# Kernel tuning notes

Measured on AMD Instinct MI355X. Metric: run time of the kernel, lower is better.

The kernel has to match this reference:

```python
import jax, jax.numpy as jnp
import numpy as np

D_MODEL, D_STATE, D_CONV, EXPAND = 1024, 64, 4, 2
D_INNER = D_MODEL * EXPAND
BATCH, SEQ = 4, 4096


def setup_inputs() -> dict:
    key = jax.random.key(0)
    ks = jax.random.split(key, 9)
    s = lambda fan_in: 1.0 / np.sqrt(fan_in)
    return {
        "x": jax.random.normal(ks[0], (BATCH, SEQ, D_MODEL), jnp.float32),
        "in_proj_w": jax.random.uniform(ks[1], (D_MODEL, 2 * D_INNER), jnp.float32, -s(D_MODEL), s(D_MODEL)),
        "conv_w": jax.random.uniform(ks[2], (D_INNER, 1, D_CONV), jnp.float32, -s(D_CONV), s(D_CONV)),
        "conv_b": jax.random.uniform(ks[3], (D_INNER,), jnp.float32, -s(D_CONV), s(D_CONV)),
        "sB_w": jax.random.uniform(ks[4], (D_INNER, D_STATE), jnp.float32, -s(D_INNER), s(D_INNER)),
        "sC_w": jax.random.uniform(ks[5], (D_INNER, D_STATE), jnp.float32, -s(D_INNER), s(D_INNER)),
        "sdelta_w": jax.random.uniform(ks[6], (D_INNER, D_INNER), jnp.float32, -s(D_INNER), s(D_INNER)),
        "sdelta_b": jax.random.uniform(ks[7], (D_INNER,), jnp.float32, -s(D_INNER), s(D_INNER)),
        "A_log": jnp.log(jnp.arange(1, D_STATE + 1, dtype=jnp.float32)),
        "D_param": jnp.ones((D_INNER,), jnp.float32),
        "out_proj_w": jax.random.uniform(ks[8], (D_INNER, D_MODEL), jnp.float32, -s(D_INNER), s(D_INNER)),
        "out_proj_b": jnp.zeros((D_MODEL,), jnp.float32),
    }


def reference(x, in_proj_w, conv_w, conv_b, sB_w, sC_w, sdelta_w, sdelta_b, A_log, D_param, out_proj_w, out_proj_b):
    batch, seq_len, _ = x.shape
    d_inner = conv_w.shape[0]
    k = conv_w.shape[-1]
    # input projection + gate split
    x_proj = x @ in_proj_w                         # (B, L, 2*Di)
    x_ssm, x_gate = jnp.split(x_proj, 2, axis=-1)
    # causal depthwise conv1d: torch pads (k-1) both sides then truncates to L == left-pad only
    xc = jnp.transpose(x_ssm, (0, 2, 1))           # (B, Di, L)
    xc = jax.lax.conv_general_dilated(
        xc, conv_w, window_strides=(1,), padding=[(k - 1, 0)],
        dimension_numbers=("NCH", "OIH", "NCH"), feature_group_count=d_inner)
    xc = xc + conv_b[None, :, None]
    xc = jax.nn.silu(jnp.transpose(xc, (0, 2, 1)))  # (B, L, Di)
    # selection mechanism
    A = -jnp.exp(A_log)                            # (N,)
    Bm = xc @ sB_w                                 # (B, L, N)
    Cm = xc @ sC_w                                 # (B, L, N)
    delta = jax.nn.softplus(xc @ sdelta_w + sdelta_b)  # (B, L, Di)
    # selective scan over time with lax.scan
    def step(h, inp):
        xt, dt, Bt, Ct = inp                       # (B,Di),(B,Di),(B,N),(B,N)
        Abar = jnp.exp(dt[..., None] * A)          # (B, Di, N)
        h = Abar * h + (dt * xt)[..., None] * Bt[:, None, :]
        y = jnp.einsum("bdn,bn->bd", h, Ct)
        return h, y
    h0 = jnp.zeros((batch, d_inner, A.shape[0]), x.dtype)
    xs = (jnp.swapaxes(xc, 0, 1), jnp.swapaxes(delta, 0, 1),
          jnp.swapaxes(Bm, 0, 1), jnp.swapaxes(Cm, 0, 1))
    _, ys = jax.lax.scan(step, h0, xs)             # (L, B, Di)
    y = jnp.swapaxes(ys, 0, 1) + xc * D_param      # skip via D
    y = y * jax.nn.silu(x_gate)                    # gating
    return y @ out_proj_w + out_proj_b             # (B, L, d_model)
```

## Files before the change

kernel.cpp:

```cpp
#include <hip/hip_runtime.h>
#include <math.h>


typedef __bf16 bf16;
typedef __attribute__((__ext_vector_type__(8))) __bf16 bf16x8;
typedef __attribute__((__ext_vector_type__(4))) __bf16 bf16x4;
typedef __attribute__((__ext_vector_type__(4))) float  f32x4;

#define DM     1024
#define DI     2048
#define NPROJ  4096
#define LSEQ   4096
#define NB     4
#define NS     64
#define NCH    32
#define TC     128

#define LDT 72

__global__ __launch_bounds__(256) void transpose_w(const float* __restrict__ in,
                                                   bf16* __restrict__ out,
                                                   int R, int C) {
  __shared__ float tile[32][33];
  int bc = blockIdx.x * 32, br = blockIdx.y * 32;
  int tx = threadIdx.x & 31, ty = threadIdx.x >> 5;
#pragma unroll
  for (int i = 0; i < 32; i += 8)
    tile[ty + i][tx] = in[(size_t)(br + ty + i) * C + bc + tx];
  __syncthreads();
#pragma unroll
  for (int i = 0; i < 32; i += 8)
    out[(size_t)(bc + ty + i) * R + br + tx] = (bf16)tile[tx][ty + i];
}

template <int EPI, int ADT>
__global__ __launch_bounds__(256) void gemm_bt(const void* __restrict__ Ap,
                                               const bf16* __restrict__ Wt,
                                               const float* __restrict__ bias,
                                               void* __restrict__ Cp,
                                               void* __restrict__ Cp2,
                                               int M, int N, int Nsplit, int K) {
  __shared__ __align__(16) bf16 As[128 * LDT];
  __shared__ __align__(16) bf16 Bs[128 * LDT];
  const int tid = threadIdx.x;
  const int m0 = blockIdx.x * 128, n0 = blockIdx.y * 128;
  const int wave = tid >> 6, lane = tid & 63;
  const int wm = (wave & 1) * 64, wn = (wave >> 1) * 64;
  const int lr = lane & 15, lq = lane >> 4;

  f32x4 acc[4][4];
  const f32x4 z4 = {0.f, 0.f, 0.f, 0.f};
#pragma unroll
  for (int i = 0; i < 4; i++)
#pragma unroll
    for (int j = 0; j < 4; j++) acc[i][j] = z4;

  for (int k0 = 0; k0 < K; k0 += 64) {
    if (ADT == 1) {
      const float* A = (const float*)Ap;
#pragma unroll
      for (int it = 0; it < 8; it++) {
        int e = tid + it * 256;
        int row = e >> 4, col4 = (e & 15) * 4;
        float4 v = *(const float4*)&A[(size_t)(m0 + row) * K + k0 + col4];
        bf16x4 t = {(bf16)v.x, (bf16)v.y, (bf16)v.z, (bf16)v.w};
        *(bf16x4*)&As[row * LDT + col4] = t;
      }
    } else {
      const bf16* A = (const bf16*)Ap;
#pragma unroll
      for (int it = 0; it < 4; it++) {
        int e = tid + it * 256;
        int row = e >> 3, col8 = (e & 7) * 8;
        bf16x8 v = *(const bf16x8*)&A[(size_t)(m0 + row) * K + k0 + col8];
        *(bf16x8*)&As[row * LDT + col8] = v;
      }
    }
#pragma unroll
    for (int it = 0; it < 4; it++) {
      int e = tid + it * 256;
      int row = e >> 3, col8 = (e & 7) * 8;
      bf16x8 v = *(const bf16x8*)&Wt[(size_t)(n0 + row) * K + k0 + col8];
      *(bf16x8*)&Bs[row * LDT + col8] = v;
    }
    __syncthreads();
#pragma unroll
    for (int kk = 0; kk < 64; kk += 32) {
      bf16x8 af[4], bfr[4];
#pragma unroll
      for (int i = 0; i < 4; i++)
        af[i] = *(const bf16x8*)&As[(wm + i * 16 + lr) * LDT + kk + lq * 8];
#pragma unroll
      for (int j = 0; j < 4; j++)
        bfr[j] = *(const bf16x8*)&Bs[(wn + j * 16 + lr) * LDT + kk + lq * 8];
#pragma unroll
      for (int i = 0; i < 4; i++)
#pragma unroll
        for (int j = 0; j < 4; j++)
          acc[i][j] = __builtin_amdgcn_mfma_f32_16x16x32_bf16(af[i], bfr[j],
                                                              acc[i][j], 0, 0, 0);
    }
    __syncthreads();
  }

#pragma unroll
  for (int i = 0; i < 4; i++) {
#pragma unroll
    for (int j = 0; j < 4; j++) {
#pragma unroll
      for (int r = 0; r < 4; r++) {
        int row = m0 + wm + i * 16 + lq * 4 + r;
        int col = n0 + wn + j * 16 + lr;
        float v = acc[i][j][r];
        if (EPI == 0) {
          if (col < Nsplit)
            ((bf16*)Cp)[(size_t)row * Nsplit + col] = (bf16)v;
          else
            ((bf16*)Cp2)[(size_t)row * (N - Nsplit) + (col - Nsplit)] = (bf16)v;
        } else if (EPI == 1) {
          v += bias[col];
          v = (v > 20.f) ? v : log1pf(__expf(v));
          ((bf16*)Cp)[(size_t)row * N + col] = (bf16)v;
        } else if (EPI == 2) {
          ((float*)Cp)[(size_t)row * N + col] = v;
        } else {
          v += bias[col];
          ((float*)Cp)[(size_t)row * N + col] = v;
        }
      }
    }
  }
}

__global__ __launch_bounds__(256) void conv_silu(const bf16* __restrict__ xssm,
                                                 const float* __restrict__ w,
                                                 const float* __restrict__ cb,
                                                 bf16* __restrict__ xc) {
  size_t idx = (size_t)blockIdx.x * 256 + threadIdx.x;
  int d = (int)(idx & (DI - 1));
  size_t bt = idx >> 11;
  int t = (int)(bt & (LSEQ - 1));
  const float4 wv = *(const float4*)&w[d * 4];
  float acc = cb[d];
  const bf16* base = xssm + bt * DI + d;
  if (t >= 3) acc += (float)base[-3 * DI] * wv.x;
  if (t >= 2) acc += (float)base[-2 * DI] * wv.y;
  if (t >= 1) acc += (float)base[-1 * DI] * wv.z;
  acc += (float)base[0] * wv.w;
  acc = acc / (1.f + __expf(-acc));
  xc[idx] = (bf16)acc;
}

__global__ __launch_bounds__(256) void scan_pass1(const bf16* __restrict__ delta,
                                                  const bf16* __restrict__ xc,
                                                  const float* __restrict__ BC,
                                                  float* __restrict__ S,
                                                  float* __restrict__ SD) {
  __shared__ __align__(16) float Bsh[64][64];
  const int b = blockIdx.z, c = blockIdx.y, d = blockIdx.x * 256 + threadIdx.x;
  const int tid = threadIdx.x;
  float h[NS];
#pragma unroll
  for (int n = 0; n < NS; n++) h[n] = 0.f;
  float sumdt = 0.f;

  for (int half = 0; half < 2; half++) {
    const int tbase = c * TC + half * 64;
    __syncthreads();
#pragma unroll
    for (int it = 0; it < 4; it++) {
      int e = tid + it * 256;
      int tt = e >> 4, n4 = (e & 15) * 4;
      *(float4*)&Bsh[tt][n4] =
          *(const float4*)&BC[((size_t)b * LSEQ + tbase + tt) * 128 + n4];
    }
    __syncthreads();
    for (int tt = 0; tt < 64; tt++) {
      size_t o = ((size_t)b * LSEQ + tbase + tt) * DI + d;
      float dt = (float)delta[o];
      float xv = (float)xc[o];
      float dx = dt * xv;
      float r = __expf(-dt);
      sumdt += dt;
      float rp = r;
#pragma unroll
      for (int n4 = 0; n4 < 16; n4++) {
        float4 Bv = *(const float4*)&Bsh[tt][n4 * 4];
        h[n4 * 4 + 0] = rp * h[n4 * 4 + 0] + dx * Bv.x; rp *= r;
        h[n4 * 4 + 1] = rp * h[n4 * 4 + 1] + dx * Bv.y; rp *= r;
        h[n4 * 4 + 2] = rp * h[n4 * 4 + 2] + dx * Bv.z; rp *= r;
        h[n4 * 4 + 3] = rp * h[n4 * 4 + 3] + dx * Bv.w; rp *= r;
      }
    }
  }
  size_t sb = (((size_t)b * NCH + c) * NS) * DI + d;
#pragma unroll
  for (int n = 0; n < NS; n++) S[sb + (size_t)n * DI] = h[n];
  SD[((size_t)b * NCH + c) * DI + d] = sumdt;
}

__global__ __launch_bounds__(256) void scan_pass2(float* __restrict__ S,
                                                  const float* __restrict__ SD) {
  const int d = blockIdx.x * 256 + threadIdx.x;
  const int n = blockIdx.y, b = blockIdx.z;
  const float nf = -(float)(n + 1);
  float h = 0.f;
  for (int c = 0; c < NCH; c++) {
    size_t o = (((size_t)b * NCH + c) * NS + n) * DI + d;
    float s = S[o];
    S[o] = h;
    float sd = SD[((size_t)b * NCH + c) * DI + d];
    h = __expf(nf * sd) * h + s;
  }
}

__global__ __launch_bounds__(256) void scan_pass3(const bf16* __restrict__ delta,
                                                  const bf16* __restrict__ xc,
                                                  const float* __restrict__ BC,
                                                  const float* __restrict__ Hin,
                                                  const bf16* __restrict__ xgate,
                                                  const float* __restrict__ Dp,
                                                  bf16* __restrict__ yg) {
  __shared__ __align__(16) float Bsh[64][64];
  __shared__ __align__(16) float Csh[64][64];
  const int b = blockIdx.z, c = blockIdx.y, d = blockIdx.x * 256 + threadIdx.x;
  const int tid = threadIdx.x;
  float h[NS];
  size_t hb = (((size_t)b * NCH + c) * NS) * DI + d;
#pragma unroll
  for (int n = 0; n < NS; n++) h[n] = Hin[hb + (size_t)n * DI];
  const float Dv = Dp[d];

  for (int half = 0; half < 2; half++) {
    const int tbase = c * TC + half * 64;
    __syncthreads();
#pragma unroll
    for (int it = 0; it < 4; it++) {
      int e = tid + it * 256;
      int tt = e >> 4, n4 = (e & 15) * 4;
      size_t rowo = ((size_t)b * LSEQ + tbase + tt) * 128;
      *(float4*)&Bsh[tt][n4] = *(const float4*)&BC[rowo + n4];
      *(float4*)&Csh[tt][n4] = *(const float4*)&BC[rowo + 64 + n4];
    }
    __syncthreads();
    for (int tt = 0; tt < 64; tt++) {
      size_t row = (size_t)b * LSEQ + tbase + tt;
      size_t o = row * DI + d;
      float dt = (float)delta[o];
      float xv = (float)xc[o];
      float dx = dt * xv;
      float r = __expf(-dt);
      float rp = r;
      float y = 0.f;
#pragma unroll
      for (int n4 = 0; n4 < 16; n4++) {
        float4 Bv = *(const float4*)&Bsh[tt][n4 * 4];
        float4 Cv = *(const float4*)&Csh[tt][n4 * 4];
        h[n4 * 4 + 0] = rp * h[n4 * 4 + 0] + dx * Bv.x; y += h[n4 * 4 + 0] * Cv.x; rp *= r;
        h[n4 * 4 + 1] = rp * h[n4 * 4 + 1] + dx * Bv.y; y += h[n4 * 4 + 1] * Cv.y; rp *= r;
        h[n4 * 4 + 2] = rp * h[n4 * 4 + 2] + dx * Bv.z; y += h[n4 * 4 + 2] * Cv.z; rp *= r;
        h[n4 * 4 + 3] = rp * h[n4 * 4 + 3] + dx * Bv.w; y += h[n4 * 4 + 3] * Cv.w; rp *= r;
      }
      y += xv * Dv;
      float g = (float)xgate[o];
      y *= g / (1.f + __expf(-g));
      yg[o] = (bf16)y;
    }
  }
}

extern "C" void kernel_launch(void* const* d_in, const int* in_sizes, int n_in,
                              void* d_out, int out_size, void* d_ws, size_t ws_size,
                              hipStream_t stream) {
  const float* x         = (const float*)d_in[0];
  const float* in_proj_w = (const float*)d_in[1];
  const float* conv_w    = (const float*)d_in[2];
  const float* conv_b    = (const float*)d_in[3];
  const float* sB_w      = (const float*)d_in[4];
  const float* sC_w      = (const float*)d_in[5];
  const float* sdelta_w  = (const float*)d_in[6];
  const float* sdelta_b  = (const float*)d_in[7];
  const float* D_param    = (const float*)d_in[9];
  const float* out_proj_w = (const float*)d_in[10];
  const float* out_proj_b = (const float*)d_in[11];
  float* out = (float*)d_out;

  char* ws = (char*)d_ws;
  size_t off = 0;
  auto alloc = [&](size_t bytes) {
    char* p = ws + off;
    off += (bytes + 255) & ~(size_t)255;
    return p;
  };
  bf16* W1t  = (bf16*)alloc((size_t)NPROJ * DM * 2);
  bf16* Wdt  = (bf16*)alloc((size_t)DI * DI * 2);
  bf16* WBCt = (bf16*)alloc((size_t)128 * DI * 2);
  bf16* Wot  = (bf16*)alloc((size_t)DM * DI * 2);
  const size_t weight_bytes = off;

  const size_t PB = (size_t)LSEQ * DI * 2
                  + (size_t)LSEQ * DI * 2
                  + (size_t)LSEQ * DI * 2
                  + (size_t)LSEQ * DI * 2
                  + (size_t)LSEQ * 128 * 4
                  + (size_t)NCH * NS * DI * 4
                  + (size_t)NCH * DI * 4
                  + 8 * 256;
  int G = (ws_size >= weight_bytes + 4 * PB) ? 4
        : (ws_size >= weight_bytes + 2 * PB) ? 2 : 1;

  bf16*  xssm  = (bf16*)alloc((size_t)G * LSEQ * DI * 2);
  bf16*  xgate = (bf16*)alloc((size_t)G * LSEQ * DI * 2);
  bf16*  xc    = (bf16*)alloc((size_t)G * LSEQ * DI * 2);
  bf16*  delta = (bf16*)alloc((size_t)G * LSEQ * DI * 2);
  float* BC    = (float*)alloc((size_t)G * LSEQ * 128 * 4);
  float* S     = (float*)alloc((size_t)G * NCH * NS * DI * 4);
  float* SD    = (float*)alloc((size_t)G * NCH * DI * 4);
  bf16*  yg    = xssm;

  transpose_w<<<dim3(NPROJ / 32, DM / 32), 256, 0, stream>>>(in_proj_w, W1t, DM, NPROJ);
  transpose_w<<<dim3(DI / 32, DI / 32), 256, 0, stream>>>(sdelta_w, Wdt, DI, DI);
  transpose_w<<<dim3(NS / 32, DI / 32), 256, 0, stream>>>(sB_w, WBCt, DI, NS);
  transpose_w<<<dim3(NS / 32, DI / 32), 256, 0, stream>>>(sC_w, WBCt + (size_t)NS * DI, DI, NS);
  transpose_w<<<dim3(DM / 32, DI / 32), 256, 0, stream>>>(out_proj_w, Wot, DI, DM);

  const int M = G * LSEQ;
  for (int g = 0; g < NB / G; g++) {
    const float* xg_in = x + (size_t)g * G * LSEQ * DM;
    float* out_g = out + (size_t)g * G * LSEQ * DM;

    gemm_bt<0, 1><<<dim3(M / 128, NPROJ / 128), 256, 0, stream>>>(
        xg_in, W1t, nullptr, xssm, xgate, M, NPROJ, DI, DM);
    conv_silu<<<((size_t)M * DI) / 256, 256, 0, stream>>>(xssm, conv_w, conv_b, xc);
    gemm_bt<1, 0><<<dim3(M / 128, DI / 128), 256, 0, stream>>>(
        xc, Wdt, sdelta_b, delta, nullptr, M, DI, DI, DI);
    gemm_bt<2, 0><<<dim3(M / 128, 1), 256, 0, stream>>>(
        xc, WBCt, nullptr, BC, nullptr, M, 128, 128, DI);
    scan_pass1<<<dim3(DI / 256, NCH, G), 256, 0, stream>>>(delta, xc, BC, S, SD);
    scan_pass2<<<dim3(DI / 256, NS, G), 256, 0, stream>>>(S, SD);
    scan_pass3<<<dim3(DI / 256, NCH, G), 256, 0, stream>>>(delta, xc, BC, S, xgate,
                                                           D_param, yg);
    gemm_bt<3, 0><<<dim3(M / 128, DM / 128), 256, 0, stream>>>(
        yg, Wot, out_proj_b, out_g, nullptr, M, DM, DM, DI);
  }
}
```

Measured before the change: 1.595 ms.

## Use direct global-to-LDS loads in GEMM, fuse delta/BC GEMMs, restructure scan decay

GEMM tile loads now go through global_load_lds straight into unpadded LDS, so the register round-trip is gone. The input x is first cast to bf16 by a separate kernel, which lets every GEMM share one bf16 A path. The delta and B/C projection GEMMs are merged into a single launch with a split epilogue (softplus to bf16 for delta, fp32 for BC). In the scan kernels the serial decay-power chain is replaced by precomputed powers stepped by r^8, and the y reduction uses four accumulators to shorten dependency chains. The unpadded LDS layout may cause bank conflicts on the fragment reads, and the extra cast pass adds memory traffic.

```diff
diff --git a/kernel.cpp b/kernel.cpp
--- a/kernel.cpp
+++ b/kernel.cpp
@@ -16,7 +16,19 @@
 #define NCH    32
 #define TC     128
 
-#define LDT 72
+__device__ __forceinline__ void gl_lds16(const bf16* g, bf16* l) {
+  __builtin_amdgcn_global_load_lds(
+      (const __attribute__((address_space(1))) void*)g,
+      (__attribute__((address_space(3))) void*)l, 16, 0, 0);
+}
+
+__global__ __launch_bounds__(256) void cast_bf16(const float* __restrict__ in,
+                                                 bf16* __restrict__ out) {
+  size_t i = ((size_t)blockIdx.x * 256 + threadIdx.x) * 4;
+  float4 v = *(const float4*)&in[i];
+  bf16x4 t = {(bf16)v.x, (bf16)v.y, (bf16)v.z, (bf16)v.w};
+  *(bf16x4*)&out[i] = t;
+}
 
 __global__ __launch_bounds__(256) void transpose_w(const float* __restrict__ in,
                                                    bf16* __restrict__ out,
@@ -33,15 +45,15 @@
     out[(size_t)(bc + ty + i) * R + br + tx] = (bf16)tile[tx][ty + i];
 }
 
-template <int EPI, int ADT>
-__global__ __launch_bounds__(256) void gemm_bt(const void* __restrict__ Ap,
+template <int EPI>
+__global__ __launch_bounds__(256) void gemm_bt(const bf16* __restrict__ A,
                                                const bf16* __restrict__ Wt,
                                                const float* __restrict__ bias,
                                                void* __restrict__ Cp,
                                                void* __restrict__ Cp2,
                                                int M, int N, int Nsplit, int K) {
-  __shared__ __align__(16) bf16 As[128 * LDT];
-  __shared__ __align__(16) bf16 Bs[128 * LDT];
+  __shared__ __align__(16) bf16 As[128 * 64];
+  __shared__ __align__(16) bf16 Bs[128 * 64];
   const int tid = threadIdx.x;
   const int m0 = blockIdx.x * 128, n0 = blockIdx.y * 128;
   const int wave = tid >> 6, lane = tid & 63;
@@ -56,32 +68,13 @@
     for (int j = 0; j < 4; j++) acc[i][j] = z4;
 
   for (int k0 = 0; k0 < K; k0 += 64) {
-    if (ADT == 1) {
-      const float* A = (const float*)Ap;
-#pragma unroll
-      for (int it = 0; it < 8; it++) {
-        int e = tid + it * 256;
-        int row = e >> 4, col4 = (e & 15) * 4;
-        float4 v = *(const float4*)&A[(size_t)(m0 + row) * K + k0 + col4];
-        bf16x4 t = {(bf16)v.x, (bf16)v.y, (bf16)v.z, (bf16)v.w};
-        *(bf16x4*)&As[row * LDT + col4] = t;
-      }
-    } else {
-      const bf16* A = (const bf16*)Ap;
-#pragma unroll
-      for (int it = 0; it < 4; it++) {
-        int e = tid + it * 256;
-        int row = e >> 3, col8 = (e & 7) * 8;
-        bf16x8 v = *(const bf16x8*)&A[(size_t)(m0 + row) * K + k0 + col8];
-        *(bf16x8*)&As[row * LDT + col8] = v;
-      }
-    }
 #pragma unroll
     for (int it = 0; it < 4; it++) {
-      int e = tid + it * 256;
-      int row = e >> 3, col8 = (e & 7) * 8;
-      bf16x8 v = *(const bf16x8*)&Wt[(size_t)(n0 + row) * K + k0 + col8];
-      *(bf16x8*)&Bs[row * LDT + col8] = v;
+      int ci = wave * 4 + it;
+      int c = ci * 64 + lane;
+      int row = c >> 3, col8 = (c & 7) * 8;
+      gl_lds16(&A[(size_t)(m0 + row) * K + k0 + col8], &As[ci * 512]);
+      gl_lds16(&Wt[(size_t)(n0 + row) * K + k0 + col8], &Bs[ci * 512]);
     }
     __syncthreads();
 #pragma unroll
@@ -89,10 +82,10 @@
       bf16x8 af[4], bfr[4];
 #pragma unroll
       for (int i = 0; i < 4; i++)
-        af[i] = *(const bf16x8*)&As[(wm + i * 16 + lr) * LDT + kk + lq * 8];
+        af[i] = *(const bf16x8*)&As[(wm + i * 16 + lr) * 64 + kk + lq * 8];
 #pragma unroll
       for (int j = 0; j < 4; j++)
-        bfr[j] = *(const bf16x8*)&Bs[(wn + j * 16 + lr) * LDT + kk + lq * 8];
+        bfr[j] = *(const bf16x8*)&Bs[(wn + j * 16 + lr) * 64 + kk + lq * 8];
 #pragma unroll
       for (int i = 0; i < 4; i++)
 #pragma unroll
@@ -117,12 +110,14 @@
             ((bf16*)Cp)[(size_t)row * Nsplit + col] = (bf16)v;
           else
             ((bf16*)Cp2)[(size_t)row * (N - Nsplit) + (col - Nsplit)] = (bf16)v;
-        } else if (EPI == 1) {
-          v += bias[col];
-          v = (v > 20.f) ? v : log1pf(__expf(v));
-          ((bf16*)Cp)[(size_t)row * N + col] = (bf16)v;
         } else if (EPI == 2) {
-          ((float*)Cp)[(size_t)row * N + col] = v;
+          if (col < Nsplit) {
+            v += bias[col];
+            v = (v > 20.f) ? v : log1pf(__expf(v));
+            ((bf16*)Cp)[(size_t)row * Nsplit + col] = (bf16)v;
+          } else {
+            ((float*)Cp2)[(size_t)row * (N - Nsplit) + (col - Nsplit)] = v;
+          }
         } else {
           v += bias[col];
           ((float*)Cp)[(size_t)row * N + col] = v;
@@ -151,6 +146,15 @@
   xc[idx] = (bf16)acc;
 }
 
+#define DECAY_POWERS(r, p)                         \
+  float r2 = (r) * (r);                            \
+  float r4 = r2 * r2;                              \
+  float r8 = r4 * r4;                              \
+  float p[8];                                      \
+  p[0] = (r);  p[1] = r2;      p[2] = r2 * (r);    \
+  p[3] = r4;   p[4] = r4 * (r); p[5] = r4 * r2;    \
+  p[6] = p[5] * (r);  p[7] = r8;
+
 __global__ __launch_bounds__(256) void scan_pass1(const bf16* __restrict__ delta,
                                                   const bf16* __restrict__ xc,
                                                   const float* __restrict__ BC,
@@ -182,14 +186,24 @@
       float dx = dt * xv;
       float r = __expf(-dt);
       sumdt += dt;
-      float rp = r;
-#pragma unroll
-      for (int n4 = 0; n4 < 16; n4++) {
-        float4 Bv = *(const float4*)&Bsh[tt][n4 * 4];
-        h[n4 * 4 + 0] = rp * h[n4 * 4 + 0] + dx * Bv.x; rp *= r;
-        h[n4 * 4 + 1] = rp * h[n4 * 4 + 1] + dx * Bv.y; rp *= r;
-        h[n4 * 4 + 2] = rp * h[n4 * 4 + 2] + dx * Bv.z; rp *= r;
-        h[n4 * 4 + 3] = rp * h[n4 * 4 + 3] + dx * Bv.w; rp *= r;
+      DECAY_POWERS(r, p)
+#pragma unroll
+      for (int g8 = 0; g8 < 8; g8++) {
+        float4 Bv0 = *(const float4*)&Bsh[tt][g8 * 8];
+        float4 Bv1 = *(const float4*)&Bsh[tt][g8 * 8 + 4];
+        int n = g8 * 8;
+        h[n + 0] = fmaf(p[0], h[n + 0], dx * Bv0.x);
+        h[n + 1] = fmaf(p[1], h[n + 1], dx * Bv0.y);
+        h[n + 2] = fmaf(p[2], h[n + 2], dx * Bv0.z);
+        h[n + 3] = fmaf(p[3], h[n + 3], dx * Bv0.w);
+        h[n + 4] = fmaf(p[4], h[n + 4], dx * Bv1.x);
+        h[n + 5] = fmaf(p[5], h[n + 5], dx * Bv1.y);
+        h[n + 6] = fmaf(p[6], h[n + 6], dx * Bv1.z);
+        h[n + 7] = fmaf(p[7], h[n + 7], dx * Bv1.w);
+        if (g8 != 7) {
+#pragma unroll
+          for (int j = 0; j < 8; j++) p[j] *= r8;
+        }
       }
     }
   }
@@ -250,17 +264,29 @@
       float xv = (float)xc[o];
       float dx = dt * xv;
       float r = __expf(-dt);
-      float rp = r;
-      float y = 0.f;
-#pragma unroll
-      for (int n4 = 0; n4 < 16; n4++) {
-        float4 Bv = *(const float4*)&Bsh[tt][n4 * 4];
-        float4 Cv = *(const float4*)&Csh[tt][n4 * 4];
-        h[n4 * 4 + 0] = rp * h[n4 * 4 + 0] + dx * Bv.x; y += h[n4 * 4 + 0] * Cv.x; rp *= r;
-        h[n4 * 4 + 1] = rp * h[n4 * 4 + 1] + dx * Bv.y; y += h[n4 * 4 + 1] * Cv.y; rp *= r;
-        h[n4 * 4 + 2] = rp * h[n4 * 4 + 2] + dx * Bv.z; y += h[n4 * 4 + 2] * Cv.z; rp *= r;
-        h[n4 * 4 + 3] = rp * h[n4 * 4 + 3] + dx * Bv.w; y += h[n4 * 4 + 3] * Cv.w; rp *= r;
+      DECAY_POWERS(r, p)
+      float y0 = 0.f, y1 = 0.f, y2 = 0.f, y3 = 0.f;
+#pragma unroll
+      for (int g8 = 0; g8 < 8; g8++) {
+        float4 Bv0 = *(const float4*)&Bsh[tt][g8 * 8];
+        float4 Bv1 = *(const float4*)&Bsh[tt][g8 * 8 + 4];
+        float4 Cv0 = *(const float4*)&Csh[tt][g8 * 8];
+        float4 Cv1 = *(const float4*)&Csh[tt][g8 * 8 + 4];
+        int n = g8 * 8;
+        h[n + 0] = fmaf(p[0], h[n + 0], dx * Bv0.x); y0 = fmaf(h[n + 0], Cv0.x, y0);
+        h[n + 1] = fmaf(p[1], h[n + 1], dx * Bv0.y); y1 = fmaf(h[n + 1], Cv0.y, y1);
+        h[n + 2] = fmaf(p[2], h[n + 2], dx * Bv0.z); y2 = fmaf(h[n + 2], Cv0.z, y2);
+        h[n + 3] = fmaf(p[3], h[n + 3], dx * Bv0.w); y3 = fmaf(h[n + 3], Cv0.w, y3);
+        h[n + 4] = fmaf(p[4], h[n + 4], dx * Bv1.x); y0 = fmaf(h[n + 4], Cv1.x, y0);
+        h[n + 5] = fmaf(p[5], h[n + 5], dx * Bv1.y); y1 = fmaf(h[n + 5], Cv1.y, y1);
+        h[n + 6] = fmaf(p[6], h[n + 6], dx * Bv1.z); y2 = fmaf(h[n + 6], Cv1.z, y2);
+        h[n + 7] = fmaf(p[7], h[n + 7], dx * Bv1.w); y3 = fmaf(h[n + 7], Cv1.w, y3);
+        if (g8 != 7) {
+#pragma unroll
+          for (int j = 0; j < 8; j++) p[j] *= r8;
+        }
       }
+      float y = (y0 + y1) + (y2 + y3);
       y += xv * Dv;
       float g = (float)xgate[o];
       y *= g / (1.f + __expf(-g));
@@ -293,10 +319,11 @@
     return p;
   };
   bf16* W1t  = (bf16*)alloc((size_t)NPROJ * DM * 2);
-  bf16* Wdt  = (bf16*)alloc((size_t)DI * DI * 2);
-  bf16* WBCt = (bf16*)alloc((size_t)128 * DI * 2);
+  bf16* WdBC = (bf16*)alloc((size_t)(DI + 128) * DI * 2);
   bf16* Wot  = (bf16*)alloc((size_t)DM * DI * 2);
-  const size_t weight_bytes = off;
+  bf16* xb   = (bf16*)alloc((size_t)NB * LSEQ * DM * 2);
+  bf16* WBCt = WdBC + (size_t)DI * DI;
+  const size_t fixed_bytes = off;
 
   const size_t PB = (size_t)LSEQ * DI * 2
                   + (size_t)LSEQ * DI * 2
@@ -306,8 +333,8 @@
                   + (size_t)NCH * NS * DI * 4
                   + (size_t)NCH * DI * 4
                   + 8 * 256;
-  int G = (ws_size >= weight_bytes + 4 * PB) ? 4
-        : (ws_size >= weight_bytes + 2 * PB) ? 2 : 1;
+  int G = (ws_size >= fixed_bytes + 4 * PB) ? 4
+        : (ws_size >= fixed_bytes + 2 * PB) ? 2 : 1;
 
   bf16*  xssm  = (bf16*)alloc((size_t)G * LSEQ * DI * 2);
   bf16*  xgate = (bf16*)alloc((size_t)G * LSEQ * DI * 2);
@@ -318,29 +345,28 @@
   float* SD    = (float*)alloc((size_t)G * NCH * DI * 4);
   bf16*  yg    = xssm;
 
+  cast_bf16<<<(NB * (size_t)LSEQ * DM) / 1024, 256, 0, stream>>>(x, xb);
   transpose_w<<<dim3(NPROJ / 32, DM / 32), 256, 0, stream>>>(in_proj_w, W1t, DM, NPROJ);
-  transpose_w<<<dim3(DI / 32, DI / 32), 256, 0, stream>>>(sdelta_w, Wdt, DI, DI);
+  transpose_w<<<dim3(DI / 32, DI / 32), 256, 0, stream>>>(sdelta_w, WdBC, DI, DI);
   transpose_w<<<dim3(NS / 32, DI / 32), 256, 0, stream>>>(sB_w, WBCt, DI, NS);
   transpose_w<<<dim3(NS / 32, DI / 32), 256, 0, stream>>>(sC_w, WBCt + (size_t)NS * DI, DI, NS);
   transpose_w<<<dim3(DM / 32, DI / 32), 256, 0, stream>>>(out_proj_w, Wot, DI, DM);
 
   const int M = G * LSEQ;
   for (int g = 0; g < NB / G; g++) {
-    const float* xg_in = x + (size_t)g * G * LSEQ * DM;
+    const bf16* xg_in = xb + (size_t)g * G * LSEQ * DM;
     float* out_g = out + (size_t)g * G * LSEQ * DM;
 
-    gemm_bt<0, 1><<<dim3(M / 128, NPROJ / 128), 256, 0, stream>>>(
+    gemm_bt<0><<<dim3(M / 128, NPROJ / 128), 256, 0, stream>>>(
         xg_in, W1t, nullptr, xssm, xgate, M, NPROJ, DI, DM);
     conv_silu<<<((size_t)M * DI) / 256, 256, 0, stream>>>(xssm, conv_w, conv_b, xc);
-    gemm_bt<1, 0><<<dim3(M / 128, DI / 128), 256, 0, stream>>>(
-        xc, Wdt, sdelta_b, delta, nullptr, M, DI, DI, DI);
-    gemm_bt<2, 0><<<dim3(M / 128, 1), 256, 0, stream>>>(
-        xc, WBCt, nullptr, BC, nullptr, M, 128, 128, DI);
+    gemm_bt<2><<<dim3(M / 128, (DI + 128) / 128), 256, 0, stream>>>(
+        xc, WdBC, sdelta_b, delta, BC, M, DI + 128, DI, DI);
     scan_pass1<<<dim3(DI / 256, NCH, G), 256, 0, stream>>>(delta, xc, BC, S, SD);
     scan_pass2<<<dim3(DI / 256, NS, G), 256, 0, stream>>>(S, SD);
     scan_pass3<<<dim3(DI / 256, NCH, G), 256, 0, stream>>>(delta, xc, BC, S, xgate,
                                                            D_param, yg);
-    gemm_bt<3, 0><<<dim3(M / 128, DM / 128), 256, 0, stream>>>(
+    gemm_bt<3><<<dim3(M / 128, DM / 128), 256, 0, stream>>>(
         yg, Wot, out_proj_b, out_g, nullptr, M, DM, DM, DI);
   }
 }
```

Result: faster. 1.487 ms (-6.8%).
